# Kernel optimization log

Hardware: AMD Instinct MI355X
Metric: run time of the kernel (lower is better)

## Reference

```python
import jax, jax.numpy as jnp
import numpy as np

B, C, N, K, COUT = 4, 64, 8192, 16, 64
EPS = 1e-5  # BatchNorm1d default eps


def setup_inputs() -> dict:
    key = jax.random.key(0)
    k1, k2, k3 = jax.random.split(key, 3)
    x = jax.random.normal(k1, (B, C, N), dtype=jnp.float32)
    coords = jax.random.normal(k2, (B, 3, N), dtype=jnp.float32)
    # Linear(2C -> COUT) params
    W = jax.random.normal(k3, (2 * C, COUT), dtype=jnp.float32) * (1.0 / np.sqrt(2 * C))
    b = jnp.zeros((COUT,), dtype=jnp.float32)
    # BatchNorm1d affine params (train-mode batch stats, as in torch default)
    gamma = jnp.ones((COUT,), dtype=jnp.float32)
    beta = jnp.zeros((COUT,), dtype=jnp.float32)
    return {"x": x, "coords": coords, "W": W, "b": b, "gamma": gamma, "beta": beta}


def reference(x, coords, W, b, gamma, beta):
    k = min(K, max(N - 1, 1))
    # --- kNN in coordinate space (squared distances give same ordering as cdist) ---
    ct = jnp.swapaxes(coords, 1, 2)                      # (B, N, 3)
    sq = jnp.sum(ct * ct, axis=-1)                       # (B, N)
    d2 = sq[:, :, None] + sq[:, None, :] - 2.0 * jnp.einsum('bnd,bmd->bnm', ct, ct)
    _, idx = jax.lax.top_k(-d2, k + 1)                   # smallest k+1 distances
    idx = idx[:, :, 1:]                                  # drop self -> (B, N, k)
    # --- gather neighbor features ---
    xt = jnp.swapaxes(x, 1, 2)                           # (B, N, C)
    nb = jax.vmap(lambda f, i: f[i])(xt, idx)            # (B, N, k, C)
    center = jnp.broadcast_to(xt[:, :, None, :], nb.shape)
    edge = jnp.concatenate([center, nb - center], axis=-1)  # (B, N, k, 2C)
    # --- edge MLP: Linear -> BatchNorm1d (batch stats) -> ReLU ---
    h = jnp.einsum('bnkc,cd->bnkd', edge, W) + b         # (B, N, k, COUT)
    mean = jnp.mean(h, axis=(0, 1, 2))
    var = jnp.var(h, axis=(0, 1, 2))
    h = (h - mean) * jax.lax.rsqrt(var + EPS) * gamma + beta
    h = jax.nn.relu(h)
    # --- max-pool over k neighbors ---
    out = jnp.max(h, axis=2)                             # (B, N, COUT)
    return jnp.swapaxes(out, 1, 2)                       # (B, COUT, N)
```

## Files before the change

kernel.cpp:

```cpp
#include <hip/hip_runtime.h>


#define Bn 4
#define Nn 8192
#define NSL 8
#define Gc 32
#define CS 32896
#define Hc 0.375f

typedef unsigned long long ull;

__device__ __forceinline__ int cellof(float v) {
  int i = (int)floorf((v + 6.0f) * (1.0f / Hc));
  return min(Gc - 1, max(0, i));
}

__global__ __launch_bounds__(256) void transpose_kernel(const float* __restrict__ x,
                                                        const float* __restrict__ coords,
                                                        float* __restrict__ xt,
                                                        float4* __restrict__ cpack) {
  __shared__ float tile[64][65];
  int bid = blockIdx.x;
  int b = bid >> 7;
  int n0 = (bid & 127) << 6;
  int tx = threadIdx.x & 63;
  int ty = threadIdx.x >> 6;
  for (int c = ty; c < 64; c += 4)
    tile[tx][c] = x[((size_t)b * 64 + c) * Nn + n0 + tx];
  if (ty == 0) {
    int n = n0 + tx;
    const float* cb = coords + (size_t)b * 3 * Nn;
    float cx = cb[n], cy = cb[Nn + n], cz = cb[2 * Nn + n];
    float cs = __fadd_rn(__fadd_rn(__fmul_rn(cx, cx), __fmul_rn(cy, cy)),
                         __fmul_rn(cz, cz));
    cpack[(size_t)b * Nn + n] = make_float4(cx, cy, cz, cs);
  }
  __syncthreads();
  for (int r = ty; r < 64; r += 4)
    xt[((size_t)b * Nn + n0 + r) * 64 + tx] = tile[r][tx];
}

__global__ __launch_bounds__(256) void hist_kernel(const float4* __restrict__ cpack,
                                                   unsigned* __restrict__ cells,
                                                   unsigned* __restrict__ cstart) {
  int n = blockIdx.x * 256 + threadIdx.x;
  float4 c = cpack[n];
  unsigned cell = ((unsigned)cellof(c.z) * Gc + cellof(c.y)) * Gc + cellof(c.x);
  cells[n] = cell;
  atomicAdd(&cstart[(unsigned)(n >> 13) * CS + cell], 1u);
}

__global__ __launch_bounds__(256) void scanA_kernel(unsigned* __restrict__ cstart,
                                                    unsigned* __restrict__ partials) {
  __shared__ unsigned sums[256];
  int bid = blockIdx.x, b = bid >> 4, ch = bid & 15, t = threadIdx.x;
  unsigned* base = cstart + (size_t)b * CS + ch * 2048 + t * 8;
  unsigned v[8], p = 0;
#pragma unroll
  for (int j = 0; j < 8; ++j) { unsigned c = base[j]; v[j] = p; p += c; }
  sums[t] = p;
  __syncthreads();
  for (int off = 1; off < 256; off <<= 1) {
    unsigned u = (t >= off) ? sums[t - off] : 0u;
    __syncthreads();
    sums[t] += u;
    __syncthreads();
  }
  unsigned excl = sums[t] - p;
#pragma unroll
  for (int j = 0; j < 8; ++j) base[j] = v[j] + excl;
  if (t == 255) partials[bid] = sums[255];
}

__global__ __launch_bounds__(256) void scanC_kernel(unsigned* __restrict__ cstart,
                                                    unsigned* __restrict__ cursor,
                                                    const unsigned* __restrict__ partials) {
  int bid = blockIdx.x, b = bid >> 4, ch = bid & 15, t = threadIdx.x;
  unsigned off = 0;
  for (int k = 0; k < ch; ++k) off += partials[b * 16 + k];
  size_t o = (size_t)b * CS + ch * 2048 + t * 8;
#pragma unroll
  for (int j = 0; j < 8; ++j) {
    unsigned val = cstart[o + j] + off;
    cstart[o + j] = val;
    cursor[o + j] = val;
  }
}

__global__ __launch_bounds__(256) void scatter_kernel(const float4* __restrict__ cpack,
                                                      const unsigned* __restrict__ cells,
                                                      unsigned* __restrict__ cursor,
                                                      float4* __restrict__ spos4,
                                                      unsigned* __restrict__ sidx) {
  int n = blockIdx.x * 256 + threadIdx.x;
  int b = n >> 13;
  unsigned slot = atomicAdd(&cursor[(size_t)b * CS + cells[n]], 1u);
  spos4[(size_t)b * Nn + slot] = cpack[n];
  sidx[(size_t)b * Nn + slot] = (unsigned)(n & 8191);
}

__global__ __launch_bounds__(256) void bbox_kernel(const float4* __restrict__ spos4,
                                                   float4* __restrict__ bbox) {
  __shared__ float4 smn[256], smx[256];
  int blk = blockIdx.x;
  int t = threadIdx.x;
  const float4* sp = spos4 + (size_t)(blk >> 4) * Nn + (blk & 15) * 512;
  float4 a = sp[t], c = sp[t + 256];
  smn[t] = make_float4(fminf(a.x, c.x), fminf(a.y, c.y), fminf(a.z, c.z), 0.f);
  smx[t] = make_float4(fmaxf(a.x, c.x), fmaxf(a.y, c.y), fmaxf(a.z, c.z), 0.f);
  __syncthreads();
  for (int off = 128; off > 0; off >>= 1) {
    if (t < off) {
      float4 n2 = smn[t + off], x2 = smx[t + off], n1 = smn[t], x1 = smx[t];
      smn[t] = make_float4(fminf(n1.x, n2.x), fminf(n1.y, n2.y), fminf(n1.z, n2.z), 0.f);
      smx[t] = make_float4(fmaxf(x1.x, x2.x), fmaxf(x1.y, x2.y), fmaxf(x1.z, x2.z), 0.f);
    }
    __syncthreads();
  }
  if (t == 0) { bbox[blk * 2] = smn[0]; bbox[blk * 2 + 1] = smx[0]; }
}

#define RMAX(kv) do {                                         \
    ull _kk = (kv);                                           \
    _Pragma("unroll")                                         \
    for (int _u = 0; _u < 16; ++_u)                           \
      ad[_u] = (ad[_u] == thr) ? _kk : ad[_u];                \
    ull _t0 = ad[0] > ad[1] ? ad[0] : ad[1];                  \
    ull _t1 = ad[2] > ad[3] ? ad[2] : ad[3];                  \
    ull _t2 = ad[4] > ad[5] ? ad[4] : ad[5];                  \
    ull _t3 = ad[6] > ad[7] ? ad[6] : ad[7];                  \
    ull _t4 = ad[8] > ad[9] ? ad[8] : ad[9];                  \
    ull _t5 = ad[10] > ad[11] ? ad[10] : ad[11];              \
    ull _t6 = ad[12] > ad[13] ? ad[12] : ad[13];              \
    ull _t7 = ad[14] > ad[15] ? ad[14] : ad[15];              \
    ull _u0 = _t0 > _t1 ? _t0 : _t1;                          \
    ull _u1 = _t2 > _t3 ? _t2 : _t3;                          \
    ull _u2 = _t4 > _t5 ? _t4 : _t5;                          \
    ull _u3 = _t6 > _t7 ? _t6 : _t7;                          \
    ull _v0 = _u0 > _u1 ? _u0 : _u1;                          \
    ull _v1 = _u2 > _u3 ? _u2 : _u3;                          \
    thr = _v0 > _v1 ? _v0 : _v1;                              \
  } while (0)

#define SINS(kv) do {                                         \
    ull _kk = (kv);                                           \
    if (_kk < nad[15]) {                                      \
      bool _ci = true;                                        \
      _Pragma("unroll")                                       \
      for (int _u = 15; _u >= 1; --_u) {                      \
        bool _cm = _kk < nad[_u - 1];                         \
        nad[_u] = _ci ? (_cm ? nad[_u - 1] : _kk) : nad[_u];  \
        _ci = _cm;                                            \
      }                                                       \
      nad[0] = _ci ? _kk : nad[0];                            \
    }                                                         \
  } while (0)

__global__ __launch_bounds__(512) void knn_kernel(const float4* __restrict__ spos4,
                                                  const unsigned* __restrict__ sidx,
                                                  const float4* __restrict__ bbox,
                                                  int* __restrict__ knn) {
  __shared__ __align__(16) ull mk[(NSL - 1) * 16 * 64];
  float4* stage = (float4*)mk;
  unsigned* sixl = (unsigned*)(mk + 1024);
  __shared__ unsigned sthr[64];

  int bid = blockIdx.x;
  int b = bid >> 7;
  int grp = bid & 127;
  int tid = threadIdx.x;
  int lane = tid & 63;
  int s = tid >> 6;
  int qslot = grp * 64 + lane;

  const float4* sp = spos4 + (size_t)b * Nn;
  const unsigned* sx = sidx + (size_t)b * Nn;

  float4 qc = sp[qslot];
  unsigned qg = sx[qslot];
  float qs = qc.w;
  float qx2 = 2.f * qc.x, qy2 = 2.f * qc.y, qz2 = 2.f * qc.z;

  if (tid < 64) sthr[tid] = 0xFFFFFFFFu;

  ull ad[16];
#pragma unroll
  for (int i = 0; i < 16; ++i) ad[i] = 0xFFFFFFFF00000000ull | (unsigned)i;
  ull thr = 0xFFFFFFFF0000000Full;
  unsigned thr_hi = 0xFFFFFFFFu;

  int m0 = grp >> 3;
  int visited = 0;
  for (int step = 0; step < 32 && visited < 16; ++step) {
    int d = (step + 1) >> 1;
    int m = (step & 1) ? (m0 + d) : (m0 - d);
    if (m < 0 || m >= 16) continue;
    ++visited;

    __syncthreads();

    float4 bmn = bbox[(b * 16 + m) * 2];
    float4 bmx = bbox[(b * 16 + m) * 2 + 1];
    float ddx = fmaxf(fmaxf(bmn.x - qc.x, qc.x - bmx.x), 0.f);
    float ddy = fmaxf(fmaxf(bmn.y - qc.y, qc.y - bmx.y), 0.f);
    float ddz = fmaxf(fmaxf(bmn.z - qc.z, qc.z - bmx.z), 0.f);
    float dmin2 = ddx * ddx + ddy * ddy + ddz * ddz;
    unsigned shu = sthr[lane];
    int skipl = (dmin2 > __uint_as_float(shu) + 1e-3f) ? 1 : 0;
    if (__all(skipl)) continue;

    stage[tid] = sp[m * 512 + tid];
    sixl[tid] = sx[m * 512 + tid];
    __syncthreads();
#pragma unroll
    for (int half = 0; half < 2; ++half) {
      int loc = half * 256 + s * 32;
      int base = m * 512 + loc;
      unsigned sh = sthr[lane];
      thr_hi = sh < thr_hi ? sh : thr_hi;
      unsigned mask = 0;
#pragma unroll 8
      for (int j = 0; j < 32; ++j) {
        float4 c4 = stage[loc + j];
        float dot2 = __fadd_rn(__fadd_rn(__fmul_rn(qx2, c4.x), __fmul_rn(qy2, c4.y)),
                               __fmul_rn(qz2, c4.z));
        float d2 = __fsub_rn(__fadd_rn(qs, c4.w), dot2);
        mask |= (__float_as_uint(d2) <= thr_hi) ? (1u << j) : 0u;
      }
      unsigned sj = (unsigned)(qslot - base);
      if (sj < 32u) mask &= ~(1u << sj);
      while (__any(mask)) {
        if (mask) {
          int j = __ffs(mask) - 1;
          mask &= (mask - 1);
          float4 c4 = stage[loc + j];
          float dot2 = __fadd_rn(__fadd_rn(__fmul_rn(qx2, c4.x), __fmul_rn(qy2, c4.y)),
                                 __fmul_rn(qz2, c4.z));
          float d2 = __fsub_rn(__fadd_rn(qs, c4.w), dot2);
          ull key = ((ull)__float_as_uint(d2) << 32) | sixl[loc + j];
          if (key < thr) RMAX(key);
        }
      }
      unsigned lh = (unsigned)(thr >> 32);
      thr_hi = lh < thr_hi ? lh : thr_hi;
      atomicMin(&sthr[lane], lh);
    }
  }

  __syncthreads();
  if (s > 0) {
#pragma unroll
    for (int i = 0; i < 16; ++i) mk[(((s - 1) << 4) + i) * 64 + lane] = ad[i];
  }
  __syncthreads();
  if (s == 0) {
    ull nad[16];
#pragma unroll
    for (int i = 0; i < 16; ++i) nad[i] = ~0ull;
#pragma unroll
    for (int i = 0; i < 16; ++i) SINS(ad[i]);
    for (int t = 0; t < (NSL - 1) * 16; ++t) SINS(mk[t * 64 + lane]);
    int* op = knn + (size_t)(b * Nn + (int)qg) * 16;
#pragma unroll
    for (int i = 0; i < 16; ++i) op[i] = (int)(nad[i] & 0xFFFFFFFFull);
  }
}

__global__ __launch_bounds__(256, 2) void edge_kernel(
    const float* __restrict__ xt, const int* __restrict__ knn,
    const float* __restrict__ W, const float* __restrict__ bias,
    float* __restrict__ mnb, float* __restrict__ mxb,
    float* __restrict__ ps1, float* __restrict__ ps2) {
  __shared__ float dlds[4][16][64];
  __shared__ float clds[4][64];
  __shared__ float r1[4][64], r2[4][64];

  int tid = threadIdx.x;
  int l = tid & 63;
  int w = tid >> 6;

  float w1[64], w2[64];
#pragma unroll
  for (int c = 0; c < 64; ++c) {
    w1[c] = W[c * 64 + l];
    w2[c] = W[(64 + c) * 64 + l];
  }
  float bl = bias[l];
  float s1 = 0.f, s2 = 0.f;

  int wid = blockIdx.x * 4 + w;
  int nw = gridDim.x * 4;
  for (int p = wid; p < Bn * Nn; p += nw) {
    int bb = p >> 13;
    const float* xb = xt + (size_t)bb * Nn * 64;
    float ctr = xt[(size_t)p * 64 + l];
    clds[w][l] = ctr;
    const int* ip = knn + (size_t)p * 16;
#pragma unroll
    for (int j = 0; j < 16; ++j) {
      int nj = ip[j];
      dlds[w][j][l] = xb[(size_t)nj * 64 + l] - ctr;
    }
    __syncthreads();

    const float4* cv = (const float4*)clds[w];
    float cc = bl;
#pragma unroll
    for (int c = 0; c < 16; ++c) {
      float4 v = cv[c];
      cc = fmaf(v.w, w1[4 * c + 3], fmaf(v.z, w1[4 * c + 2],
           fmaf(v.y, w1[4 * c + 1], fmaf(v.x, w1[4 * c + 0], cc))));
    }

    float mn = 3.0e38f, mx = -3.0e38f;
#pragma unroll
    for (int k = 0; k < 16; ++k) {
      const float4* dv = (const float4*)dlds[w][k];
      float h = cc;
#pragma unroll
      for (int c = 0; c < 16; ++c) {
        float4 v = dv[c];
        h = fmaf(v.w, w2[4 * c + 3], fmaf(v.z, w2[4 * c + 2],
            fmaf(v.y, w2[4 * c + 1], fmaf(v.x, w2[4 * c + 0], h))));
      }
      mn = fminf(mn, h);
      mx = fmaxf(mx, h);
      s1 += h;
      s2 = fmaf(h, h, s2);
    }
    mnb[(size_t)p * 64 + l] = mn;
    mxb[(size_t)p * 64 + l] = mx;
    __syncthreads();
  }

  r1[w][l] = s1; r2[w][l] = s2;
  __syncthreads();
  if (w == 0) {
    float a = r1[0][l] + r1[1][l] + r1[2][l] + r1[3][l];
    float c2 = r2[0][l] + r2[1][l] + r2[2][l] + r2[3][l];
    ps1[blockIdx.x * 64 + l] = a;
    ps2[blockIdx.x * 64 + l] = c2;
  }
}

__global__ __launch_bounds__(256) void stats_kernel(const float* __restrict__ ps1,
                                                    const float* __restrict__ ps2,
                                                    float* __restrict__ stats) {
  __shared__ float r1[4][64], r2[4][64];
  int c = threadIdx.x & 63, g = threadIdx.x >> 6;
  float a = 0.f, b2 = 0.f;
  for (int i = g; i < 512; i += 4) { a += ps1[i * 64 + c]; b2 += ps2[i * 64 + c]; }
  r1[g][c] = a; r2[g][c] = b2;
  __syncthreads();
  if (g == 0) {
    float s1 = r1[0][c] + r1[1][c] + r1[2][c] + r1[3][c];
    float s2 = r2[0][c] + r2[1][c] + r2[2][c] + r2[3][c];
    const float invM = 1.f / 524288.f;
    float mean = s1 * invM;
    float var = s2 * invM - mean * mean;
    stats[c] = mean;
    stats[64 + c] = var;
  }
}

__global__ __launch_bounds__(256) void final_kernel(
    const float* __restrict__ mnb, const float* __restrict__ mxb,
    const float* __restrict__ stats, const float* __restrict__ gamma,
    const float* __restrict__ beta, float* __restrict__ out) {
  __shared__ float tile[64][65];
  int bid = blockIdx.x;
  int b = bid >> 7;
  int n0 = (bid & 127) << 6;
  int tx = threadIdx.x & 63, ty = threadIdx.x >> 6;
  float mean = stats[tx], var = stats[64 + tx];
  float sc = gamma[tx] * rsqrtf(var + 1e-5f);
  float sh = fmaf(-mean, sc, beta[tx]);
  for (int r = ty; r < 64; r += 4) {
    size_t off = ((size_t)(b * Nn + n0 + r)) * 64 + tx;
    float lo = fmaf(mnb[off], sc, sh);
    float hi = fmaf(mxb[off], sc, sh);
    tile[tx][r] = fmaxf(fmaxf(hi, lo), 0.f);
  }
  __syncthreads();
  for (int r = ty; r < 64; r += 4)
    out[((size_t)b * 64 + r) * Nn + n0 + tx] = tile[r][tx];
}

extern "C" void kernel_launch(void* const* d_in, const int* in_sizes, int n_in,
                              void* d_out, int out_size, void* d_ws, size_t ws_size,
                              hipStream_t stream) {
  const float* x      = (const float*)d_in[0];
  const float* coords = (const float*)d_in[1];
  const float* W      = (const float*)d_in[2];
  const float* bias   = (const float*)d_in[3];
  const float* gamma  = (const float*)d_in[4];
  const float* beta   = (const float*)d_in[5];
  float* out = (float*)d_out;

  char* ws = (char*)d_ws;
  float*    xt       = (float*)ws;
  int*      knn      = (int*)(ws + 8388608);
  float*    mnb      = (float*)(ws + 10485760);
  float4*   cpack    = (float4*)(ws + 10485760);
  float*    mxb      = (float*)(ws + 18874368);
  float4*   spos4    = (float4*)(ws + 18874368);
  unsigned* cstart   = (unsigned*)(ws + 19398656);
  unsigned* cursor   = (unsigned*)(ws + 19924992);
  unsigned* cells    = (unsigned*)(ws + 20451328);
  unsigned* partials = (unsigned*)(ws + 20582400);
  unsigned* sidx     = (unsigned*)(ws + 20582656);
  float4*   bbox     = (float4*)(ws + 20713728);
  float*    ps1      = (float*)(ws + 27262976);
  float*    ps2      = (float*)(ws + 27394048);
  float*    stats    = (float*)(ws + 27525120);

  transpose_kernel<<<dim3(512), dim3(256), 0, stream>>>(x, coords, xt, cpack);
  hipMemsetAsync(cstart, 0, (size_t)4 * CS * 4, stream);
  hist_kernel<<<dim3(128), dim3(256), 0, stream>>>(cpack, cells, cstart);
  scanA_kernel<<<dim3(64), dim3(256), 0, stream>>>(cstart, partials);
  scanC_kernel<<<dim3(64), dim3(256), 0, stream>>>(cstart, cursor, partials);
  scatter_kernel<<<dim3(128), dim3(256), 0, stream>>>(cpack, cells, cursor, spos4, sidx);
  bbox_kernel<<<dim3(64), dim3(256), 0, stream>>>(spos4, bbox);
  knn_kernel<<<dim3(512), dim3(512), 0, stream>>>(spos4, sidx, bbox, knn);
  edge_kernel<<<dim3(512), dim3(256), 0, stream>>>(xt, knn, W, bias, mnb, mxb, ps1, ps2);
  stats_kernel<<<dim3(1), dim3(256), 0, stream>>>(ps1, ps2, stats);
  final_kernel<<<dim3(512), dim3(256), 0, stream>>>(mnb, mxb, stats, gamma, beta, out);
}
```

Measured before the change: 590.5 us.

## Remap kNN kernel to 32 queries per block with half-wave splitting

The kNN kernel now handles 32 queries per 256-thread block instead of 64 queries per 512-thread block, launching 1024 blocks. Each wave is split into two half-waves that scan different 32-candidate slices for the same queries, which keeps the 8-way candidate split. The staging loads and the final merge are reworked to fit the new lane mapping. This gives more, smaller blocks, which may improve load balance and occupancy, but candidate tiles are loaded twice as often per query and the per-lane branches in the insert loop now diverge at half-wave granularity.

```diff
diff --git a/kernel.cpp b/kernel.cpp
--- a/kernel.cpp
+++ b/kernel.cpp
@@ -3,7 +3,6 @@
 
 #define Bn 4
 #define Nn 8192
-#define NSL 8
 #define Gc 32
 #define CS 32896
 #define Hc 0.375f
@@ -156,22 +155,24 @@
     }                                                         \
   } while (0)
 
-__global__ __launch_bounds__(512) void knn_kernel(const float4* __restrict__ spos4,
+__global__ __launch_bounds__(256) void knn_kernel(const float4* __restrict__ spos4,
                                                   const unsigned* __restrict__ sidx,
                                                   const float4* __restrict__ bbox,
                                                   int* __restrict__ knn) {
-  __shared__ __align__(16) ull mk[(NSL - 1) * 16 * 64];
+  __shared__ __align__(16) ull mk[7 * 16 * 32];
   float4* stage = (float4*)mk;
   unsigned* sixl = (unsigned*)(mk + 1024);
-  __shared__ unsigned sthr[64];
+  __shared__ unsigned sthr[32];
 
   int bid = blockIdx.x;
-  int b = bid >> 7;
-  int grp = bid & 127;
+  int b = bid >> 8;
+  int grp = bid & 255;
   int tid = threadIdx.x;
   int lane = tid & 63;
+  int l32 = lane & 31;
   int s = tid >> 6;
-  int qslot = grp * 64 + lane;
+  int ss = (s << 1) | (lane >> 5);
+  int qslot = grp * 32 + l32;
 
   const float4* sp = spos4 + (size_t)b * Nn;
   const unsigned* sx = sidx + (size_t)b * Nn;
@@ -181,7 +182,7 @@
   float qs = qc.w;
   float qx2 = 2.f * qc.x, qy2 = 2.f * qc.y, qz2 = 2.f * qc.z;
 
-  if (tid < 64) sthr[tid] = 0xFFFFFFFFu;
+  if (tid < 32) sthr[tid] = 0xFFFFFFFFu;
 
   ull ad[16];
 #pragma unroll
@@ -189,7 +190,7 @@
   ull thr = 0xFFFFFFFF0000000Full;
   unsigned thr_hi = 0xFFFFFFFFu;
 
-  int m0 = grp >> 3;
+  int m0 = grp >> 4;
   int visited = 0;
   for (int step = 0; step < 32 && visited < 16; ++step) {
     int d = (step + 1) >> 1;
@@ -205,18 +206,20 @@
     float ddy = fmaxf(fmaxf(bmn.y - qc.y, qc.y - bmx.y), 0.f);
     float ddz = fmaxf(fmaxf(bmn.z - qc.z, qc.z - bmx.z), 0.f);
     float dmin2 = ddx * ddx + ddy * ddy + ddz * ddz;
-    unsigned shu = sthr[lane];
+    unsigned shu = sthr[l32];
     int skipl = (dmin2 > __uint_as_float(shu) + 1e-3f) ? 1 : 0;
     if (__all(skipl)) continue;
 
     stage[tid] = sp[m * 512 + tid];
+    stage[tid + 256] = sp[m * 512 + 256 + tid];
     sixl[tid] = sx[m * 512 + tid];
+    sixl[tid + 256] = sx[m * 512 + 256 + tid];
     __syncthreads();
 #pragma unroll
     for (int half = 0; half < 2; ++half) {
-      int loc = half * 256 + s * 32;
+      int loc = half * 256 + ss * 32;
       int base = m * 512 + loc;
-      unsigned sh = sthr[lane];
+      unsigned sh = sthr[l32];
       thr_hi = sh < thr_hi ? sh : thr_hi;
       unsigned mask = 0;
 #pragma unroll 8
@@ -243,23 +246,28 @@
       }
       unsigned lh = (unsigned)(thr >> 32);
       thr_hi = lh < thr_hi ? lh : thr_hi;
-      atomicMin(&sthr[lane], lh);
+      atomicMin(&sthr[l32], lh);
     }
   }
 
   __syncthreads();
-  if (s > 0) {
-#pragma unroll
-    for (int i = 0; i < 16; ++i) mk[(((s - 1) << 4) + i) * 64 + lane] = ad[i];
-  }
-  __syncthreads();
-  if (s == 0) {
+  if (lane >= 32) {
+    int row = 2 * s;
+#pragma unroll
+    for (int i = 0; i < 16; ++i) mk[(row * 16 + i) * 32 + l32] = ad[i];
+  } else if (s > 0) {
+    int row = 2 * s - 1;
+#pragma unroll
+    for (int i = 0; i < 16; ++i) mk[(row * 16 + i) * 32 + l32] = ad[i];
+  }
+  __syncthreads();
+  if (s == 0 && lane < 32) {
     ull nad[16];
 #pragma unroll
     for (int i = 0; i < 16; ++i) nad[i] = ~0ull;
 #pragma unroll
     for (int i = 0; i < 16; ++i) SINS(ad[i]);
-    for (int t = 0; t < (NSL - 1) * 16; ++t) SINS(mk[t * 64 + lane]);
+    for (int t = 0; t < 7 * 16; ++t) SINS(mk[t * 32 + l32]);
     int* op = knn + (size_t)(b * Nn + (int)qg) * 16;
 #pragma unroll
     for (int i = 0; i < 16; ++i) op[i] = (int)(nad[i] & 0xFFFFFFFFull);
@@ -421,7 +429,7 @@
   scanC_kernel<<<dim3(64), dim3(256), 0, stream>>>(cstart, cursor, partials);
   scatter_kernel<<<dim3(128), dim3(256), 0, stream>>>(cpack, cells, cursor, spos4, sidx);
   bbox_kernel<<<dim3(64), dim3(256), 0, stream>>>(spos4, bbox);
-  knn_kernel<<<dim3(512), dim3(512), 0, stream>>>(spos4, sidx, bbox, knn);
+  knn_kernel<<<dim3(1024), dim3(256), 0, stream>>>(spos4, sidx, bbox, knn);
   edge_kernel<<<dim3(512), dim3(256), 0, stream>>>(xt, knn, W, bias, mnb, mxb, ps1, ps2);
   stats_kernel<<<dim3(1), dim3(256), 0, stream>>>(ps1, ps2, stats);
   final_kernel<<<dim3(512), dim3(256), 0, stream>>>(mnb, mxb, stats, gamma, beta, out);
```

Result: faster. 571.7 us (-3.2%).
